# Kernel optimization log

Measured on AMD Instinct MI355X. Metric: run time of the kernel, lower is better.

## Reference

```python
import jax, jax.numpy as jnp
import numpy as np

B, T, H, N = 4, 512, 32, 64
D = H * N  # n_embd = 2048


def setup_inputs() -> dict:
    key = jax.random.key(0)
    ks = jax.random.split(key, 8)
    f = lambda kk: jax.random.normal(kk, (B, T, H, N), dtype=jnp.float32)
    r = f(ks[0])
    w = f(ks[1])
    k = f(ks[2])
    v = f(ks[3])
    iclr = f(ks[4])
    # int8-style quantized output projection: int values in [-128,127] + per-row scale
    w_out_q = jax.random.randint(ks[5], (D, D), -128, 128, dtype=jnp.int32)
    w_out_scale = jax.random.uniform(ks[6], (D,), dtype=jnp.float32) * 0.01
    return {"r": r, "w": w, "k": k, "v": v, "iclr": iclr,
            "w_out_q": w_out_q, "w_out_scale": w_out_scale}


def _wkv7(r, w, k, v, iclr):
    """RWKV x070 WKV scan. All inputs [B,T,H,N]; returns [B,T,H*N]."""
    decay = jnp.exp(-jnp.exp(w))  # per-channel decay in (0,1), x070 parameterization
    # kk = l2-normalized key direction; a = -kk (removal), b = kk * sigmoid(iclr) (write)
    kk = k * jax.lax.rsqrt(jnp.sum(k * k, axis=-1, keepdims=True) + 1e-12)
    a = -kk
    b = kk * jax.nn.sigmoid(iclr)

    def step(state, inp):
        # state: [B,H,N,N]; each inp element: [B,H,N]
        r_t, d_t, k_t, v_t, a_t, b_t = inp
        sa = jnp.einsum('bhij,bhj->bhi', state, a_t)
        state = (state * d_t[:, :, None, :]
                 + sa[..., None] * b_t[:, :, None, :]
                 + v_t[..., None] * k_t[:, :, None, :])
        y_t = jnp.einsum('bhij,bhj->bhi', state, r_t)
        return state, y_t

    tb = lambda x: jnp.swapaxes(x, 0, 1)  # [B,T,H,N] -> [T,B,H,N]
    state0 = jnp.zeros((B, H, N, N), dtype=r.dtype)
    _, y = jax.lax.scan(step, state0, (tb(r), tb(decay), tb(k), tb(v), tb(a), tb(b)))
    return jnp.swapaxes(y, 0, 1).reshape(B, T, H * N)


def reference(r, w, k, v, iclr, w_out_q, w_out_scale):
    y = _wkv7(r, w, k, v, iclr)               # [B,T,D]
    # inline dequant of quantized output projection (per-output-row scale)
    W = w_out_q.astype(jnp.float32) * w_out_scale[:, None]  # [D,D]
    return jnp.einsum('btd,od->bto', y, W)    # [B,T,D]
```

## Files before the change

### kernel.cpp

```cpp
#include <hip/hip_runtime.h>
#include <hip/hip_bf16.h>
#include <stdint.h>

#define B_ 4
#define T_ 512
#define H_ 32
#define N_ 64
#define D_ 2048
#define M_ (B_*T_)

typedef __attribute__((ext_vector_type(4))) float f32x4;
typedef __attribute__((ext_vector_type(8))) short short8;

template <int CTRL>
__device__ __forceinline__ float dpp_add(float x) {
    int t = __builtin_amdgcn_mov_dpp(__float_as_int(x), CTRL, 0xF, 0xF, true);
    return x + __int_as_float(t);
}
__device__ __forceinline__ float bfly16(float x) {
    x = dpp_add<0xB1>(x);
    x = dpp_add<0x4E>(x);
    x = dpp_add<0x141>(x);
    x = dpp_add<0x140>(x);
    return x;
}

__device__ __forceinline__ void gld16(const float* g, float* l) {
    __builtin_amdgcn_global_load_lds(
        (const __attribute__((address_space(1))) unsigned int*)g,
        (__attribute__((address_space(3))) unsigned int*)l, 16, 0, 0);
}

__global__ __launch_bounds__(256) void prep(
    const float* __restrict__ r, const float* __restrict__ w,
    const float* __restrict__ k, const float* __restrict__ v,
    const float* __restrict__ iclr, float* __restrict__ pk) {
    int g = blockIdx.x * 4 + (threadIdx.x >> 6);
    int lane = threadIdx.x & 63;
    int b = g >> 14;
    int t = (g >> 5) & (T_ - 1);
    int h = g & 31;
    size_t si = (size_t)g * 64 + lane;
    size_t di = (((size_t)(b * H_ + h) * T_) + t) * 384 + lane;
    float rv = r[si], wv = w[si], kv = k[si], vv = v[si], av = iclr[si];
    float d = expf(-expf(wv));
    float ss = kv * kv;
#pragma unroll
    for (int m = 1; m < 64; m <<= 1) ss += __shfl_xor(ss, m, 64);
    float kkv = kv * rsqrtf(ss + 1e-12f);
    float bbv = kkv * (1.f / (1.f + expf(-av)));
    pk[di          ] = rv;
    pk[di + 1 * 64 ] = kv;
    pk[di + 2 * 64 ] = vv;
    pk[di + 3 * 64 ] = d;
    pk[di + 4 * 64 ] = kkv;
    pk[di + 5 * 64 ] = bbv;
}

struct Frag {
    f32x4 R, Kk, Dd, Aa, Bb;
    float v;
};

__device__ __forceinline__ Frag ldfrag(const float* rb, int jg, int row) {
    Frag f;
    f.R  = *(const f32x4*)(rb + 0 * 64 + jg * 4);
    f.Kk = *(const f32x4*)(rb + 1 * 64 + jg * 4);
    f.v  = rb[2 * 64 + row];
    f.Dd = *(const f32x4*)(rb + 3 * 64 + jg * 4);
    f.Aa = *(const f32x4*)(rb + 4 * 64 + jg * 4);
    f.Bb = *(const f32x4*)(rb + 5 * 64 + jg * 4);
    return f;
}

__global__ __launch_bounds__(64, 2) void wkv_scan(
    const float* __restrict__ pk, __hip_bfloat16* __restrict__ y,
    const int* __restrict__ q, __hip_bfloat16* __restrict__ o) {
    if (blockIdx.x >= 2048) {
        int i = ((blockIdx.x - 2048) * 64 + (int)threadIdx.x) * 4;
        int4 qi = *(const int4*)(q + i);
        __hip_bfloat16 t[4];
        t[0] = __float2bfloat16((float)qi.x);
        t[1] = __float2bfloat16((float)qi.y);
        t[2] = __float2bfloat16((float)qi.z);
        t[3] = __float2bfloat16((float)qi.w);
        *(uint2*)(o + i) = *(uint2*)t;
        return;
    }
    const int bh = blockIdx.x & 127;
    const int wv = blockIdx.x >> 7;
    const int b = bh >> 5, h = bh & 31;
    const int lane = threadIdx.x;
    const int jg = lane & 15;
    const int rl = lane >> 4;
    const int row = wv * 4 + rl;

    __shared__ __align__(16) float ring[2 * 1536];

    const float* src = pk + (size_t)bh * T_ * 384;

#pragma unroll
    for (int gg = 0; gg < 2; ++gg) {
        const float* g0 = src + (size_t)gg * 1536 + lane * 4;
        float* l0 = &ring[gg * 1536];
#pragma unroll
        for (int c = 0; c < 6; ++c)
            gld16(g0 + c * 256, l0 + c * 256);
    }

    asm volatile("s_waitcnt vmcnt(6)" ::: "memory");
    Frag cur = ldfrag(&ring[0], jg, row);
    float S[4] = {0.f, 0.f, 0.f, 0.f};

    for (int g = 0; g < T_ / 4; ++g) {
        const float* rb0 = &ring[(g & 1) * 1536];
        const float* nb0 = &ring[((g + 1) & 1) * 1536];
#pragma unroll
        for (int i = 0; i < 4; ++i) {
            Frag nxt;
            if (i < 3) {
                nxt = ldfrag(rb0 + (i + 1) * 384, jg, row);
            } else {
                asm volatile("s_waitcnt vmcnt(3)" ::: "memory");
                nxt = ldfrag(nb0, jg, row);
            }

            float s01 = fmaf(S[1], cur.Aa[1], S[0] * cur.Aa[0]);
            float s23 = fmaf(S[3], cur.Aa[3], S[2] * cur.Aa[2]);
            const float sa = -bfly16(s01 + s23);

            float t0 = fmaf(sa, cur.Bb[0], cur.v * cur.Kk[0]);
            S[0] = fmaf(S[0], cur.Dd[0], t0);
            float t1 = fmaf(sa, cur.Bb[1], cur.v * cur.Kk[1]);
            S[1] = fmaf(S[1], cur.Dd[1], t1);
            float y01 = fmaf(S[1], cur.R[1], S[0] * cur.R[0]);
            float t2 = fmaf(sa, cur.Bb[2], cur.v * cur.Kk[2]);
            S[2] = fmaf(S[2], cur.Dd[2], t2);
            float t3 = fmaf(sa, cur.Bb[3], cur.v * cur.Kk[3]);
            S[3] = fmaf(S[3], cur.Dd[3], t3);
            float y23 = fmaf(S[3], cur.R[3], S[2] * cur.R[2]);
            float ys = bfly16(y01 + y23);
            if (jg == 0)
                y[((size_t)b * T_ + (g * 4 + i)) * D_ + h * 64 + row] =
                    __float2bfloat16(ys);
            cur = nxt;
        }

        asm volatile("" ::: "memory");
        int gp = g + 2; if (gp > T_ / 4 - 1) gp = T_ / 4 - 1;
        const float* g0 = src + (size_t)gp * 1536 + lane * 4;
        float* l0 = &ring[(g & 1) * 1536];
#pragma unroll
        for (int c = 0; c < 6; ++c)
            gld16(g0 + c * 256, l0 + c * 256);
    }
}

__device__ __forceinline__ void gload_lds16(const __hip_bfloat16* g, ushort* l) {
    __builtin_amdgcn_global_load_lds(
        (const __attribute__((address_space(1))) unsigned int*)g,
        (__attribute__((address_space(3))) unsigned int*)l, 16, 0, 0);
}

__global__ __launch_bounds__(256, 2) void gemm_bt(
    const __hip_bfloat16* __restrict__ A,
    const __hip_bfloat16* __restrict__ Bq,
    const float* __restrict__ scale,
    float* __restrict__ C) {
    const int K = D_;
    __shared__ __align__(16) ushort As[128 * 64];
    __shared__ __align__(16) ushort Bs[64 * 64];

    const int tid = threadIdx.x;
    const int lane = tid & 63;
    const int wave = tid >> 6;
    const int wr = wave >> 1, wc = wave & 1;
    const int m0 = blockIdx.x * 128;
    const int n0 = blockIdx.y * 64;

    const int srow8 = lane >> 3;
    const int scol8 = (lane & 7) * 8;
    const int ml = lane & 15;
    const int kq = (lane >> 4) * 8;

    f32x4 acc[4][2] = {};

    for (int k0 = 0; k0 < K; k0 += 64) {
#pragma unroll
        for (int c = 0; c < 4; ++c) {
            int ra = wave * 32 + c * 8;
            gload_lds16(A + (size_t)(m0 + ra + srow8) * K + k0 + scol8,
                        &As[ra * 64]);
        }
#pragma unroll
        for (int c = 0; c < 2; ++c) {
            int rb = wave * 16 + c * 8;
            gload_lds16(Bq + (size_t)(n0 + rb + srow8) * K + k0 + scol8,
                        &Bs[rb * 64]);
        }
        __syncthreads();
#pragma unroll
        for (int ks = 0; ks < 2; ++ks) {
            short8 af[4], bf[2];
#pragma unroll
            for (int tm = 0; tm < 4; ++tm)
                af[tm] = *(const short8*)(&As[(wr * 64 + tm * 16 + ml) * 64 + ks * 32 + kq]);
#pragma unroll
            for (int tn = 0; tn < 2; ++tn)
                bf[tn] = *(const short8*)(&Bs[(wc * 32 + tn * 16 + ml) * 64 + ks * 32 + kq]);
#pragma unroll
            for (int tm = 0; tm < 4; ++tm)
#pragma unroll
                for (int tn = 0; tn < 2; ++tn)
                    acc[tm][tn] = __builtin_amdgcn_mfma_f32_16x16x32_bf16(
                        af[tm], bf[tn], acc[tm][tn], 0, 0, 0);
        }
        __syncthreads();
    }

#pragma unroll
    for (int tn = 0; tn < 2; ++tn) {
        int gn = n0 + wc * 32 + tn * 16 + ml;
        float sc = scale[gn];
#pragma unroll
        for (int tm = 0; tm < 4; ++tm) {
            int gm = m0 + wr * 64 + tm * 16 + (lane >> 4) * 4;
#pragma unroll
            for (int rg = 0; rg < 4; ++rg)
                C[(size_t)(gm + rg) * D_ + gn] = acc[tm][tn][rg] * sc;
        }
    }
}

extern "C" void kernel_launch(void* const* d_in, const int* in_sizes, int n_in,
                              void* d_out, int out_size, void* d_ws, size_t ws_size,
                              hipStream_t stream) {
    (void)in_sizes; (void)n_in; (void)out_size; (void)ws_size;
    const float* r  = (const float*)d_in[0];
    const float* w  = (const float*)d_in[1];
    const float* k  = (const float*)d_in[2];
    const float* v  = (const float*)d_in[3];
    const float* ic = (const float*)d_in[4];
    const int*   wq = (const int*)d_in[5];
    const float* sc = (const float*)d_in[6];
    float* out = (float*)d_out;

    char* p = (char*)d_ws;
    __hip_bfloat16* yb = (__hip_bfloat16*)p;  p += (size_t)M_ * D_ * 2;
    __hip_bfloat16* wb = (__hip_bfloat16*)p;  p += (size_t)D_ * D_ * 2;
    float* pk = (float*)p;

    prep    <<<dim3(16384), dim3(256), 0, stream>>>(r, w, k, v, ic, pk);
    wkv_scan<<<dim3(2048 + 16384), dim3(64), 0, stream>>>(pk, yb, wq, wb);
    gemm_bt <<<dim3(M_ / 128, D_ / 64), dim3(256), 0, stream>>>(yb, wb, sc, out);
}
```

Measured before the change: 282.9 us.

## Double-buffer WKV scan LDS fragment reads with inline-asm two-step pipelining

```diff
diff --git a/kernel.cpp b/kernel.cpp
--- a/kernel.cpp
+++ b/kernel.cpp
@@ -62,15 +62,43 @@
     float v;
 };
 
-__device__ __forceinline__ Frag ldfrag(const float* rb, int jg, int row) {
-    Frag f;
-    f.R  = *(const f32x4*)(rb + 0 * 64 + jg * 4);
-    f.Kk = *(const f32x4*)(rb + 1 * 64 + jg * 4);
-    f.v  = rb[2 * 64 + row];
-    f.Dd = *(const f32x4*)(rb + 3 * 64 + jg * 4);
-    f.Aa = *(const f32x4*)(rb + 4 * 64 + jg * 4);
-    f.Bb = *(const f32x4*)(rb + 5 * 64 + jg * 4);
-    return f;
+#define ISSUE_FRAG(F, a0, a1)                                   \
+    asm volatile(                                               \
+        "ds_read_b128 %0, %6 offset:1024\n\t"                   \
+        "ds_read_b128 %1, %6 offset:1280\n\t"                   \
+        "ds_read_b128 %2, %6 offset:0\n\t"                      \
+        "ds_read_b128 %3, %6 offset:256\n\t"                    \
+        "ds_read_b128 %4, %6 offset:768\n\t"                    \
+        "ds_read_b32  %5, %7"                                   \
+        : "+v"(F.Aa), "+v"(F.Bb), "+v"(F.R), "+v"(F.Kk),        \
+          "+v"(F.Dd), "+v"(F.v)                                 \
+        : "v"(a0), "v"(a1))
+
+#define TIE_FRAG(F)                                             \
+    asm volatile("s_waitcnt lgkmcnt(6)"                         \
+        : "+v"(F.Aa), "+v"(F.Bb), "+v"(F.R), "+v"(F.Kk),        \
+          "+v"(F.Dd), "+v"(F.v) :: "memory")
+
+__device__ __forceinline__ void step_c(float S[4], const Frag& F,
+                                       __hip_bfloat16* __restrict__ y,
+                                       int b, int h, int t, int jg, int row) {
+    float s01 = fmaf(S[1], F.Aa[1], S[0] * F.Aa[0]);
+    float s23 = fmaf(S[3], F.Aa[3], S[2] * F.Aa[2]);
+    const float sa = -bfly16(s01 + s23);
+
+    float t0 = fmaf(sa, F.Bb[0], F.v * F.Kk[0]);
+    S[0] = fmaf(S[0], F.Dd[0], t0);
+    float t1 = fmaf(sa, F.Bb[1], F.v * F.Kk[1]);
+    S[1] = fmaf(S[1], F.Dd[1], t1);
+    float y01 = fmaf(S[1], F.R[1], S[0] * F.R[0]);
+    float t2 = fmaf(sa, F.Bb[2], F.v * F.Kk[2]);
+    S[2] = fmaf(S[2], F.Dd[2], t2);
+    float t3 = fmaf(sa, F.Bb[3], F.v * F.Kk[3]);
+    S[3] = fmaf(S[3], F.Dd[3], t3);
+    float y23 = fmaf(S[3], F.R[3], S[2] * F.R[2]);
+    float ys = bfly16(y01 + y23);
+    if (jg == 0)
+        y[((size_t)b * T_ + t) * D_ + h * 64 + row] = __float2bfloat16(ys);
 }
 
 __global__ __launch_bounds__(64, 2) void wkv_scan(
@@ -108,51 +136,48 @@
             gld16(g0 + c * 256, l0 + c * 256);
     }
 
+    const unsigned base3 =
+        (unsigned)(size_t)(__attribute__((address_space(3))) char*)ring;
+    const unsigned avv = base3 + jg * 16;
+    const unsigned avs = base3 + 512 + row * 4;
+
     asm volatile("s_waitcnt vmcnt(6)" ::: "memory");
-    Frag cur = ldfrag(&ring[0], jg, row);
+
+    Frag FA = {}, FB = {};
+    ISSUE_FRAG(FA, avv, avs);
+    ISSUE_FRAG(FB, avv + 1536, avs + 1536);
+    TIE_FRAG(FA);
+
     float S[4] = {0.f, 0.f, 0.f, 0.f};
 
-    for (int g = 0; g < T_ / 4; ++g) {
-        const float* rb0 = &ring[(g & 1) * 1536];
-        const float* nb0 = &ring[((g + 1) & 1) * 1536];
-#pragma unroll
-        for (int i = 0; i < 4; ++i) {
-            Frag nxt;
-            if (i < 3) {
-                nxt = ldfrag(rb0 + (i + 1) * 384, jg, row);
-            } else {
-                asm volatile("s_waitcnt vmcnt(3)" ::: "memory");
-                nxt = ldfrag(nb0, jg, row);
-            }
-
-            float s01 = fmaf(S[1], cur.Aa[1], S[0] * cur.Aa[0]);
-            float s23 = fmaf(S[3], cur.Aa[3], S[2] * cur.Aa[2]);
-            const float sa = -bfly16(s01 + s23);
-
-            float t0 = fmaf(sa, cur.Bb[0], cur.v * cur.Kk[0]);
-            S[0] = fmaf(S[0], cur.Dd[0], t0);
-            float t1 = fmaf(sa, cur.Bb[1], cur.v * cur.Kk[1]);
-            S[1] = fmaf(S[1], cur.Dd[1], t1);
-            float y01 = fmaf(S[1], cur.R[1], S[0] * cur.R[0]);
-            float t2 = fmaf(sa, cur.Bb[2], cur.v * cur.Kk[2]);
-            S[2] = fmaf(S[2], cur.Dd[2], t2);
-            float t3 = fmaf(sa, cur.Bb[3], cur.v * cur.Kk[3]);
-            S[3] = fmaf(S[3], cur.Dd[3], t3);
-            float y23 = fmaf(S[3], cur.R[3], S[2] * cur.R[2]);
-            float ys = bfly16(y01 + y23);
-            if (jg == 0)
-                y[((size_t)b * T_ + (g * 4 + i)) * D_ + h * 64 + row] =
-                    __float2bfloat16(ys);
-            cur = nxt;
-        }
-
-        asm volatile("" ::: "memory");
-        int gp = g + 2; if (gp > T_ / 4 - 1) gp = T_ / 4 - 1;
-        const float* g0 = src + (size_t)gp * 1536 + lane * 4;
-        float* l0 = &ring[(g & 1) * 1536];
-#pragma unroll
-        for (int c = 0; c < 6; ++c)
-            gld16(g0 + c * 256, l0 + c * 256);
+    for (int p = 0; p < 256; ++p) {
+        const int s0 = 2 * p;
+        step_c(S, FA, y, b, h, s0, jg, row);
+
+        if (p & 1)
+            asm volatile("s_waitcnt vmcnt(3)" ::: "memory");
+
+        int s2 = s0 + 2; if (s2 > T_ - 1) s2 = T_ - 1;
+        unsigned o2 = ((unsigned)((s2 >> 2) & 1)) * 6144 + (unsigned)(s2 & 3) * 1536;
+        ISSUE_FRAG(FA, avv + o2, avs + o2);
+        TIE_FRAG(FB);
+
+        step_c(S, FB, y, b, h, s0 + 1, jg, row);
+
+        if (p & 1) {
+            const int g = (s0 + 1) >> 2;
+            int gp = g + 2; if (gp > T_ / 4 - 1) gp = T_ / 4 - 1;
+            const float* g0 = src + (size_t)gp * 1536 + lane * 4;
+            float* l0 = &ring[(g & 1) * 1536];
+#pragma unroll
+            for (int c = 0; c < 6; ++c)
+                gld16(g0 + c * 256, l0 + c * 256);
+        }
+
+        int s3 = s0 + 3; if (s3 > T_ - 1) s3 = T_ - 1;
+        unsigned o3 = ((unsigned)((s3 >> 2) & 1)) * 6144 + (unsigned)(s3 & 3) * 1536;
+        ISSUE_FRAG(FB, avv + o3, avs + o3);
+        TIE_FRAG(FA);
     }
 }
 
```

Result: slower. 299.3 us (+5.8%).
